# Optimization experiments

Measured on AMD Instinct MI355X. Metric: run time of the kernel, lower is better.

Reference implementation:

```python
import jax, jax.numpy as jnp
import numpy as np
from jax import lax

K = 3      # kernel_size
PAD = 1    # padding
OG = 2     # offset groups


def _conv2d(x, w, b):
    y = lax.conv_general_dilated(x, w, (1, 1), [(PAD, PAD), (PAD, PAD)],
                                 dimension_numbers=('NCHW', 'OIHW', 'NCHW'))
    return y + b[None, :, None, None]


def _deform_conv2d(x, offset, mask, weight):
    # torchvision-style modulated deform_conv2d (v2), stride=1, dilation=1,
    # zero out-of-bounds, offset layout [B, OG*K*K*2, H, W] with (dy, dx) pairs.
    B, C, H, W = x.shape
    O = weight.shape[0]
    K2 = K * K
    Cg = C // OG

    ki, kj = jnp.meshgrid(jnp.arange(K), jnp.arange(K), indexing='ij')
    ki = ki.reshape(K2)
    kj = kj.reshape(K2)
    base_y = jnp.arange(H)[None, :] - PAD + ki[:, None]   # [K2, H]
    base_x = jnp.arange(W)[None, :] - PAD + kj[:, None]   # [K2, W]

    off = offset.reshape(B, OG, K2, 2, H, W)
    py = off[:, :, :, 0] + base_y[None, None, :, :, None].astype(x.dtype)  # [B,OG,K2,H,W]
    px = off[:, :, :, 1] + base_x[None, None, :, None, :].astype(x.dtype)
    m = mask.reshape(B, OG, K2, H, W)

    y0f = jnp.floor(py)
    x0f = jnp.floor(px)
    wy1 = py - y0f   # bilinear weights, grads flow through py/px
    wx1 = px - x0f
    y0 = y0f.astype(jnp.int32)
    x0 = x0f.astype(jnp.int32)
    y1 = y0 + 1
    x1 = x0 + 1

    img = x.reshape(B, OG, Cg, H * W)

    def gather(yi, xi):
        valid = (yi >= 0) & (yi < H) & (xi >= 0) & (xi < W)
        idx = jnp.clip(yi, 0, H - 1) * W + jnp.clip(xi, 0, W - 1)          # [B,OG,K2,H,W]
        v = jnp.take_along_axis(img[:, :, :, None, :],
                                idx.reshape(B, OG, 1, K2, H * W), axis=-1)
        return v.reshape(B, OG, Cg, K2, H, W) * valid[:, :, None].astype(x.dtype)

    v00 = gather(y0, x0)
    v01 = gather(y0, x1)
    v10 = gather(y1, x0)
    v11 = gather(y1, x1)

    wy1e = wy1[:, :, None]   # [B,OG,1,K2,H,W]
    wx1e = wx1[:, :, None]
    val = (v00 * (1 - wy1e) * (1 - wx1e)
           + v01 * (1 - wy1e) * wx1e
           + v10 * wy1e * (1 - wx1e)
           + v11 * wy1e * wx1e)
    val = val * m[:, :, None]                               # modulation mask

    wr = weight.reshape(O, OG, Cg, K2)
    return jnp.einsum('ogck,bgckhw->bohw', wr, val)


def setup_inputs() -> dict:
    key = jax.random.key(0)
    k1, k2, k3, k4, k5 = jax.random.split(key, 5)
    B, C, O, H, W = 4, 64, 64, 128, 128
    K2 = K * K
    x = jax.random.normal(k1, (B, C, H, W), dtype=jnp.float32)
    w_main = jax.random.normal(k2, (O, C, K, K), dtype=jnp.float32) / np.sqrt(C * K2)
    w_off = jax.random.normal(k3, (2 * OG * K2, C, K, K), dtype=jnp.float32) * 0.01
    b_off = jax.random.normal(k4, (2 * OG * K2,), dtype=jnp.float32) * 0.01
    w_mask = jnp.full((OG * K2, C, K, K), 0.5, dtype=jnp.float32)  # init_mask = 0.5
    b_mask = jax.random.normal(k5, (OG * K2,), dtype=jnp.float32) * 0.01
    return {"x": x, "w_main": w_main, "w_off": w_off, "b_off": b_off,
            "w_mask": w_mask, "b_mask": b_mask}


def reference(x, w_main, w_off, b_off, w_mask, b_mask):
    offset = _conv2d(x, w_off, b_off)
    mask = jax.nn.sigmoid(_conv2d(x, w_mask, b_mask))
    return _deform_conv2d(x, offset, mask, w_main)
```

## Files before the change

### kernel.cpp

```cpp
#include <hip/hip_runtime.h>
#include <math.h>

#define BB 4
#define C 64
#define O 64
#define H 128
#define W 128
#define K2 9
#define HW (H*W)
#define NOFF 36

typedef __bf16 bf16;
typedef bf16 bf16x8 __attribute__((ext_vector_type(8)));
typedef float f32x4 __attribute__((ext_vector_type(4)));
typedef unsigned short u16x8 __attribute__((ext_vector_type(8)));
typedef unsigned int u32x4 __attribute__((ext_vector_type(4)));

#define BSTR 55
#define B2STR 19
#define VSTR 36
#define SSTR 72
#define VAL_OFF 14688
#define SMEM_BYTES 28512
#define WFRAG 18432
#define NW_TOTAL 73728

__device__ inline unsigned short f2h_bits(float f) {
  _Float16 h = (_Float16)f;
  return __builtin_bit_cast(unsigned short, h);
}
__device__ inline float h2f(unsigned short u) {
  return (float)__builtin_bit_cast(_Float16, u);
}

__global__ __launch_bounds__(256) void prep_all(
    const float* __restrict__ x, const float* __restrict__ w_main,
    const float* __restrict__ w_off, const float* __restrict__ w_mask,
    unsigned short* __restrict__ xT16, bf16* __restrict__ wfC,
    bf16* __restrict__ wfM) {
  __shared__ float tile[64][68];
  int tid = threadIdx.x;
  int b = blockIdx.x >> 8;
  int p0 = (blockIdx.x & 255) * 64;
#pragma unroll
  for (int it = 0; it < 4; ++it) {
    int c = it * 16 + (tid >> 4);
    int p4 = (tid & 15) * 4;
    *(f32x4*)&tile[c][p4] =
        *(const f32x4*)(x + (size_t)(b * C + c) * HW + p0 + p4);
  }
  __syncthreads();
#pragma unroll
  for (int it = 0; it < 2; ++it) {
    int t = it * 256 + tid;
    int p = t >> 3;
    int h8 = t & 7;
    u16x8 o;
#pragma unroll
    for (int j = 0; j < 8; ++j) {
      bf16 v = (bf16)tile[h8 * 8 + j][p];
      o[j] = __builtin_bit_cast(unsigned short, v);
    }
    *(u16x8*)&xT16[(size_t)(b * HW + p0 + p) * C + h8 * 8] = o;
  }
  int i = blockIdx.x * 256 + tid;
  if (i < NW_TOTAL) {
    int which = (i >= 36864);
    int ii = which ? i - 36864 : i;
    int j = ii & 7;
    int l = (ii >> 3) & 63;
    int rest = ii >> 9;
    int to = rest & 3;
    int kk = (rest >> 2) % 9;
    int ph = (rest >> 2) / 9;
    int m = to * 16 + (l & 15);
    int u = kk * 32 + (l >> 4) * 8 + j;
    int tap = u >> 5;
    int c1 = u & 31;
    if (!which) {
      int c = ph * 32 + c1;
      float v = (m < NOFF) ? w_off[(m * C + c) * K2 + tap]
                : (m < 54) ? w_mask[((m - NOFF) * C + c) * K2 + tap]
                           : 0.f;
      wfC[ii] = (bf16)v;
    } else {
      wfM[ii] = (bf16)w_main[(m * C + ph * 32 + c1) * K2 + tap];
    }
  }
}

__global__ __launch_bounds__(256, 5) void fused_deform(
    const bf16* __restrict__ xT, const bf16* __restrict__ wfC,
    const bf16* __restrict__ wfM, const float* __restrict__ b_off,
    const float* __restrict__ b_mask, float* __restrict__ out) {
  __shared__ __align__(16) char smem[SMEM_BYTES];
  bf16* stage = (bf16*)smem;
  float* bufF = (float*)smem;
  u32x4* buf2 = (u32x4*)smem;
  float* valF = (float*)smem;
  bf16* val = (bf16*)(smem + VAL_OFF);

  const int tid = threadIdx.x;
  const int lane = tid & 63;
  const int wv = tid >> 6;
  const int n16 = lane & 15;
  const int q4 = lane >> 4;
  const int nt = wv & 1;
  const int mh = wv >> 1;
  const int row = nt * 16 + n16;
  const int pg = tid >> 3;
  const int ch = tid & 7;

  const int g8 = blockIdx.x & 7;
  const int slot = blockIdx.x >> 3;
  const int b = g8 >> 1;
  const int ti = (g8 & 1) * 256 + slot;
  const int h0 = ti >> 2;
  const int w0 = (ti & 3) * 32;
  const bf16* xb = xT + (size_t)b * HW * C;

  bf16x8 zero8;
#pragma unroll
  for (int j = 0; j < 8; ++j) zero8[j] = (bf16)0.f;

#pragma unroll
  for (int it = 0; it < 4; ++it) {
    int id = it * 256 + tid;
    if (id < 816) {
      int chk = id & 7;
      int rest = id >> 3;
      int wp = rest % 34;
      int r = rest / 34;
      int yy = h0 + r - 1;
      int xx = w0 + wp - 1;
      bf16x8 v = zero8;
      if ((unsigned)yy < (unsigned)H && (unsigned)xx < (unsigned)W)
        v = *(const bf16x8*)(xb + (size_t)((yy << 7) + xx) * C + chk * 8);
      *(bf16x8*)(stage + (r * 34 + wp) * SSTR + chk * 8) = v;
    }
  }
  __syncthreads();
  f32x4 accC[2] = {{0.f,0.f,0.f,0.f},{0.f,0.f,0.f,0.f}};
#pragma unroll 1
  for (int ph = 0; ph < 2; ++ph) {
#pragma unroll
    for (int kk = 0; kk < 9; ++kk) {
      bf16x8 bfr = *(const bf16x8*)(stage +
          ((kk / 3) * 34 + row + kk % 3) * SSTR + ph * 32 + q4 * 8);
#pragma unroll
      for (int i = 0; i < 2; ++i) {
        int to = 2 * mh + i;
        bf16x8 afr = *(const bf16x8*)(wfC +
            (size_t)(((ph * 9 + kk) * 4 + to) * 64 + lane) * 8);
        accC[i] = __builtin_amdgcn_mfma_f32_16x16x32_bf16(afr, bfr, accC[i], 0, 0, 0);
      }
    }
  }
  __syncthreads();

#pragma unroll
  for (int i = 0; i < 2; ++i)
#pragma unroll
    for (int r = 0; r < 4; ++r) {
      int o = (2 * mh + i) * 16 + q4 * 4 + r;
      float a = accC[i][r];
      if (o < NOFF) {
        bufF[row * BSTR + o] = a + b_off[o];
      } else if (o < 54) {
        float s = a + b_mask[o - NOFF];
        bufF[row * BSTR + o] = 1.f / (1.f + __expf(-s));
      }
    }
  __syncthreads();

  unsigned int rW0[3], rW1[3], rCo[3];
#pragma unroll
  for (int it = 0; it < 3; ++it) {
    int t = it * 256 + tid;
    if (t < 576) {
      int p = t & 31;
      int gk = t >> 5;
      int g = gk / 9, tap = gk % 9;
      float offy = bufF[p * BSTR + 2 * gk];
      float offx = bufF[p * BSTR + 2 * gk + 1];
      float m = bufF[p * BSTR + NOFF + gk];
      float py = offy + (float)(h0 + tap / 3 - 1);
      float px = offx + (float)(w0 + p + tap % 3 - 1);
      float y0f = floorf(py), x0f = floorf(px);
      float wy1 = py - y0f, wx1 = px - x0f;
      float wy0 = 1.f - wy1, wx0 = 1.f - wx1;
      int y0 = (int)y0f, x0 = (int)x0f;
      int y1 = y0 + 1, x1 = x0 + 1;
      bool y0ok = (unsigned)y0 < (unsigned)H, y1ok = (unsigned)y1 < (unsigned)H;
      bool x0ok = (unsigned)x0 < (unsigned)W, x1ok = (unsigned)x1 < (unsigned)W;
      float w00 = (y0ok && x0ok) ? wy0 * wx0 * m : 0.f;
      float w01 = (y0ok && x1ok) ? wy0 * wx1 * m : 0.f;
      float w10 = (y1ok && x0ok) ? wy1 * wx0 * m : 0.f;
      float w11 = (y1ok && x1ok) ? wy1 * wx1 * m : 0.f;
      unsigned int y0c = (unsigned)min(max(y0, 0), H - 1);
      unsigned int y1c = (unsigned)min(max(y1, 0), H - 1);
      unsigned int x0c = (unsigned)min(max(x0, 0), W - 1);
      unsigned int x1c = (unsigned)min(max(x1, 0), W - 1);
      rW0[it] = (unsigned)f2h_bits(w00) | ((unsigned)f2h_bits(w01) << 16);
      rW1[it] = (unsigned)f2h_bits(w10) | ((unsigned)f2h_bits(w11) << 16);
      rCo[it] = y0c | (x0c << 8) | (y1c << 16) | (x1c << 24);
    }
  }
  __syncthreads();
#pragma unroll
  for (int it = 0; it < 3; ++it) {
    int t = it * 256 + tid;
    if (t < 576) {
      int p = t & 31;
      int gk = t >> 5;
      u32x4 pk = {rW0[it], rW1[it], rCo[it], 0u};
      buf2[p * B2STR + gk] = pk;
    }
  }
  __syncthreads();

  f32x4 accM[2] = {{0.f,0.f,0.f,0.f},{0.f,0.f,0.f,0.f}};
  const bf16* bb = xb + ch * 8;
  const int gg = ch >> 2;
#pragma unroll 1
  for (int kc = 0; kc < 3; ++kc) {
    if (kc) __syncthreads();
#pragma unroll
    for (int t = 0; t < 3; ++t) {
      int tap = kc * 3 + t;
      u32x4 t4 = buf2[pg * B2STR + gg * 9 + tap];
      float w00 = h2f(t4.x & 0xffff), w01 = h2f(t4.x >> 16);
      float w10 = h2f(t4.y & 0xffff), w11 = h2f(t4.y >> 16);
      int r0 = (int)(t4.z & 255) << 7;
      int x0 = (int)((t4.z >> 8) & 255);
      int r1 = (int)((t4.z >> 16) & 255) << 7;
      int x1 = (int)(t4.z >> 24);
      bf16x8 v00 = *(const bf16x8*)(bb + (size_t)(r0 + x0) * C);
      bf16x8 v01 = *(const bf16x8*)(bb + (size_t)(r0 + x1) * C);
      bf16x8 v10 = *(const bf16x8*)(bb + (size_t)(r1 + x0) * C);
      bf16x8 v11 = *(const bf16x8*)(bb + (size_t)(r1 + x1) * C);
      bf16x8 res;
#pragma unroll
      for (int j = 0; j < 8; ++j) {
        float v = (float)v00[j] * w00 + (float)v01[j] * w01 +
                  (float)v10[j] * w10 + (float)v11[j] * w11;
        res[j] = (bf16)v;
      }
      *(bf16x8*)(val + (t * 32 + pg) * SSTR + ch * 8) = res;
    }
    __syncthreads();
#pragma unroll
    for (int t = 0; t < 3; ++t) {
      int tap = kc * 3 + t;
#pragma unroll
      for (int g = 0; g < 2; ++g) {
        bf16x8 bfr = *(const bf16x8*)(val +
            (t * 32 + row) * SSTR + g * 32 + q4 * 8);
#pragma unroll
        for (int i = 0; i < 2; ++i) {
          int to = 2 * mh + i;
          bf16x8 afr = *(const bf16x8*)(wfM + (size_t)g * WFRAG +
              (size_t)((tap * 4 + to) * 64 + lane) * 8);
          accM[i] = __builtin_amdgcn_mfma_f32_16x16x32_bf16(afr, bfr, accM[i], 0, 0, 0);
        }
      }
    }
  }

  __syncthreads();
#pragma unroll
  for (int i = 0; i < 2; ++i)
#pragma unroll
    for (int r = 0; r < 4; ++r)
      valF[((2 * mh + i) * 16 + q4 * 4 + r) * VSTR + row] = accM[i][r];
  __syncthreads();
  {
    float* ob = out + (size_t)b * O * HW + (h0 << 7) + w0;
#pragma unroll
    for (int it = 0; it < 2; ++it) {
      int id = it * 256 + tid;
      int o = id >> 3, seg = id & 7;
      f32x4 v = *(f32x4*)&valF[o * VSTR + seg * 4];
      *(f32x4*)&ob[(size_t)o * HW + seg * 4] = v;
    }
  }
}

extern "C" void kernel_launch(void* const* d_in, const int* in_sizes, int n_in,
                              void* d_out, int out_size, void* d_ws,
                              size_t ws_size, hipStream_t stream) {
  const float* x = (const float*)d_in[0];
  const float* w_main = (const float*)d_in[1];
  const float* w_off = (const float*)d_in[2];
  const float* b_off = (const float*)d_in[3];
  const float* w_mask = (const float*)d_in[4];
  const float* b_mask = (const float*)d_in[5];
  float* out = (float*)d_out;

  unsigned short* xT16 = (unsigned short*)d_ws;
  bf16* wfC = (bf16*)(xT16 + (size_t)BB * HW * C);
  bf16* wfM = wfC + 36864;

  prep_all<<<1024, 256, 0, stream>>>(x, w_main, w_off, w_mask, xT16, wfC, wfM);
  fused_deform<<<2048, 256, 0, stream>>>((const bf16*)xT16, wfC, wfM, b_off,
                                         b_mask, out);
}
```

Measured before the change: 115.8 us.

## Shrink shared memory, write outputs directly, and raise occupancy to six blocks

The bilinear tap buffer now lives in its own region after the value staging area, so tap records are written straight to LDS. This removes the register hold and one barrier. The LDS transpose of the output tile is dropped in favour of direct scalar stores from the MFMA accumulators. Together these cut LDS use, which allows launch bounds to rise from five to six blocks per CU. The trade-off is that output stores become 4-byte accesses with 64B contiguity per row instead of 16-byte vector stores, and the new buf2 region must not overlap bufF or stage while they are still live.

```diff
diff --git a/kernel.cpp b/kernel.cpp
--- a/kernel.cpp
+++ b/kernel.cpp
@@ -18,10 +18,9 @@
 
 #define BSTR 55
 #define B2STR 19
-#define VSTR 36
 #define SSTR 72
-#define VAL_OFF 14688
-#define SMEM_BYTES 28512
+#define BUF2_OFF 13824
+#define SMEM_BYTES 23552
 #define WFRAG 18432
 #define NW_TOTAL 73728
 
@@ -89,16 +88,15 @@
   }
 }
 
-__global__ __launch_bounds__(256, 5) void fused_deform(
+__global__ __launch_bounds__(256, 6) void fused_deform(
     const bf16* __restrict__ xT, const bf16* __restrict__ wfC,
     const bf16* __restrict__ wfM, const float* __restrict__ b_off,
     const float* __restrict__ b_mask, float* __restrict__ out) {
   __shared__ __align__(16) char smem[SMEM_BYTES];
   bf16* stage = (bf16*)smem;
   float* bufF = (float*)smem;
-  u32x4* buf2 = (u32x4*)smem;
-  float* valF = (float*)smem;
-  bf16* val = (bf16*)(smem + VAL_OFF);
+  bf16* val = (bf16*)smem;
+  u32x4* buf2 = (u32x4*)(smem + BUF2_OFF);
 
   const int tid = threadIdx.x;
   const int lane = tid & 63;
@@ -173,7 +171,6 @@
     }
   __syncthreads();
 
-  unsigned int rW0[3], rW1[3], rCo[3];
 #pragma unroll
   for (int it = 0; it < 3; ++it) {
     int t = it * 256 + tid;
@@ -201,19 +198,11 @@
       unsigned int y1c = (unsigned)min(max(y1, 0), H - 1);
       unsigned int x0c = (unsigned)min(max(x0, 0), W - 1);
       unsigned int x1c = (unsigned)min(max(x1, 0), W - 1);
-      rW0[it] = (unsigned)f2h_bits(w00) | ((unsigned)f2h_bits(w01) << 16);
-      rW1[it] = (unsigned)f2h_bits(w10) | ((unsigned)f2h_bits(w11) << 16);
-      rCo[it] = y0c | (x0c << 8) | (y1c << 16) | (x1c << 24);
-    }
-  }
-  __syncthreads();
-#pragma unroll
-  for (int it = 0; it < 3; ++it) {
-    int t = it * 256 + tid;
-    if (t < 576) {
-      int p = t & 31;
-      int gk = t >> 5;
-      u32x4 pk = {rW0[it], rW1[it], rCo[it], 0u};
+      u32x4 pk;
+      pk.x = (unsigned)f2h_bits(w00) | ((unsigned)f2h_bits(w01) << 16);
+      pk.y = (unsigned)f2h_bits(w10) | ((unsigned)f2h_bits(w11) << 16);
+      pk.z = y0c | (x0c << 8) | (y1c << 16) | (x1c << 24);
+      pk.w = 0u;
       buf2[p * B2STR + gk] = pk;
     }
   }
@@ -267,22 +256,15 @@
     }
   }
 
-  __syncthreads();
-#pragma unroll
-  for (int i = 0; i < 2; ++i)
-#pragma unroll
-    for (int r = 0; r < 4; ++r)
-      valF[((2 * mh + i) * 16 + q4 * 4 + r) * VSTR + row] = accM[i][r];
-  __syncthreads();
   {
-    float* ob = out + (size_t)b * O * HW + (h0 << 7) + w0;
-#pragma unroll
-    for (int it = 0; it < 2; ++it) {
-      int id = it * 256 + tid;
-      int o = id >> 3, seg = id & 7;
-      f32x4 v = *(f32x4*)&valF[o * VSTR + seg * 4];
-      *(f32x4*)&ob[(size_t)o * HW + seg * 4] = v;
-    }
+    float* ob = out + (size_t)b * O * HW + (h0 << 7) + w0 + row;
+#pragma unroll
+    for (int i = 0; i < 2; ++i)
+#pragma unroll
+      for (int r = 0; r < 4; ++r) {
+        int o = (2 * mh + i) * 16 + q4 * 4 + r;
+        ob[(size_t)o * HW] = accM[i][r];
+      }
   }
 }
 
```

After: 117.3 us. Within noise of the previous version (+1.3%).

## Software-pipeline bilinear gathers across tap chunks and use LDS-only barriers

Applied to the files above, without the earlier changes.

Gathers for the next chunk of three taps are prefetched into registers while the current chunk is interpolated and fed to MFMAs, so global load latency overlaps compute. A lighter barrier waits only on LDS counters (lgkmcnt) instead of all outstanding memory, so pending global prefetches do not stall the barrier. The cost is 12 extra bf16x8 registers per thread, which raises VGPR pressure and may lower occupancy.

```diff
diff --git a/kernel.cpp b/kernel.cpp
--- a/kernel.cpp
+++ b/kernel.cpp
@@ -31,6 +31,12 @@
 }
 __device__ inline float h2f(unsigned short u) {
   return (float)__builtin_bit_cast(_Float16, u);
+}
+
+__device__ inline void bar_lds() {
+  asm volatile("s_waitcnt lgkmcnt(0)" ::: "memory");
+  __builtin_amdgcn_s_barrier();
+  asm volatile("" ::: "memory");
 }
 
 __global__ __launch_bounds__(256) void prep_all(
@@ -222,33 +228,60 @@
   f32x4 accM[2] = {{0.f,0.f,0.f,0.f},{0.f,0.f,0.f,0.f}};
   const bf16* bb = xb + ch * 8;
   const int gg = ch >> 2;
+
+  bf16x8 pre[12];
+  unsigned int pwx[3], pwy[3];
+#pragma unroll
+  for (int t = 0; t < 3; ++t) {
+    u32x4 t4 = buf2[pg * B2STR + gg * 9 + t];
+    pwx[t] = t4.x;
+    pwy[t] = t4.y;
+    int r0 = (int)(t4.z & 255) << 7;
+    int x0 = (int)((t4.z >> 8) & 255);
+    int r1 = (int)((t4.z >> 16) & 255) << 7;
+    int x1 = (int)(t4.z >> 24);
+    pre[t * 4 + 0] = *(const bf16x8*)(bb + (size_t)(r0 + x0) * C);
+    pre[t * 4 + 1] = *(const bf16x8*)(bb + (size_t)(r0 + x1) * C);
+    pre[t * 4 + 2] = *(const bf16x8*)(bb + (size_t)(r1 + x0) * C);
+    pre[t * 4 + 3] = *(const bf16x8*)(bb + (size_t)(r1 + x1) * C);
+  }
 #pragma unroll 1
   for (int kc = 0; kc < 3; ++kc) {
-    if (kc) __syncthreads();
+    bf16x8 res[3];
 #pragma unroll
     for (int t = 0; t < 3; ++t) {
-      int tap = kc * 3 + t;
-      u32x4 t4 = buf2[pg * B2STR + gg * 9 + tap];
-      float w00 = h2f(t4.x & 0xffff), w01 = h2f(t4.x >> 16);
-      float w10 = h2f(t4.y & 0xffff), w11 = h2f(t4.y >> 16);
-      int r0 = (int)(t4.z & 255) << 7;
-      int x0 = (int)((t4.z >> 8) & 255);
-      int r1 = (int)((t4.z >> 16) & 255) << 7;
-      int x1 = (int)(t4.z >> 24);
-      bf16x8 v00 = *(const bf16x8*)(bb + (size_t)(r0 + x0) * C);
-      bf16x8 v01 = *(const bf16x8*)(bb + (size_t)(r0 + x1) * C);
-      bf16x8 v10 = *(const bf16x8*)(bb + (size_t)(r1 + x0) * C);
-      bf16x8 v11 = *(const bf16x8*)(bb + (size_t)(r1 + x1) * C);
-      bf16x8 res;
+      float w00 = h2f(pwx[t] & 0xffff), w01 = h2f(pwx[t] >> 16);
+      float w10 = h2f(pwy[t] & 0xffff), w11 = h2f(pwy[t] >> 16);
+      bf16x8 v00 = pre[t * 4 + 0], v01 = pre[t * 4 + 1];
+      bf16x8 v10 = pre[t * 4 + 2], v11 = pre[t * 4 + 3];
 #pragma unroll
       for (int j = 0; j < 8; ++j) {
         float v = (float)v00[j] * w00 + (float)v01[j] * w01 +
                   (float)v10[j] * w10 + (float)v11[j] * w11;
-        res[j] = (bf16)v;
-      }
-      *(bf16x8*)(val + (t * 32 + pg) * SSTR + ch * 8) = res;
-    }
-    __syncthreads();
+        res[t][j] = (bf16)v;
+      }
+    }
+    if (kc < 2) {
+#pragma unroll
+      for (int t = 0; t < 3; ++t) {
+        u32x4 t4 = buf2[pg * B2STR + gg * 9 + (kc + 1) * 3 + t];
+        pwx[t] = t4.x;
+        pwy[t] = t4.y;
+        int r0 = (int)(t4.z & 255) << 7;
+        int x0 = (int)((t4.z >> 8) & 255);
+        int r1 = (int)((t4.z >> 16) & 255) << 7;
+        int x1 = (int)(t4.z >> 24);
+        pre[t * 4 + 0] = *(const bf16x8*)(bb + (size_t)(r0 + x0) * C);
+        pre[t * 4 + 1] = *(const bf16x8*)(bb + (size_t)(r0 + x1) * C);
+        pre[t * 4 + 2] = *(const bf16x8*)(bb + (size_t)(r1 + x0) * C);
+        pre[t * 4 + 3] = *(const bf16x8*)(bb + (size_t)(r1 + x1) * C);
+      }
+    }
+    if (kc) bar_lds();
+#pragma unroll
+    for (int t = 0; t < 3; ++t)
+      *(bf16x8*)(val + (t * 32 + pg) * SSTR + ch * 8) = res[t];
+    bar_lds();
 #pragma unroll
     for (int t = 0; t < 3; ++t) {
       int tap = kc * 3 + t;
```

After: 174.8 us. +51.0%, slower.

## Software-pipeline deformable gathers one tap-chunk ahead and use LDS-only barriers

Applied to the files above, without the earlier changes.

Prefetches the next three taps' bilinear corner gathers from global memory into registers while the current chunk is interpolated and fed to MFMA. This hides gather latency behind compute. It also replaces __syncthreads with a barrier that waits only on LDS counters, so the in-flight global loads are not drained at each barrier. In exchange it holds 12 extra bf16x8 registers per thread, which may strain the 5-waves launch bound and cause spills.

```diff
diff --git a/kernel.cpp b/kernel.cpp
--- a/kernel.cpp
+++ b/kernel.cpp
@@ -31,6 +31,12 @@
 }
 __device__ inline float h2f(unsigned short u) {
   return (float)__builtin_bit_cast(_Float16, u);
+}
+
+__device__ inline void bar_lds() {
+  asm volatile("s_waitcnt lgkmcnt(0)" ::: "memory");
+  __builtin_amdgcn_s_barrier();
+  asm volatile("" ::: "memory");
 }
 
 __global__ __launch_bounds__(256) void prep_all(
@@ -88,6 +94,32 @@
     }
   }
 }
+
+#define LOADTAP(GK, WX, WY, V0, V1, V2, V3)                    \
+  do {                                                         \
+    u32x4 t4 = buf2[pg * B2STR + (GK)];                        \
+    WX = t4.x;                                                 \
+    WY = t4.y;                                                 \
+    int r0 = (int)(t4.z & 255) << 7;                           \
+    int x0 = (int)((t4.z >> 8) & 255);                         \
+    int r1 = (int)((t4.z >> 16) & 255) << 7;                   \
+    int x1 = (int)(t4.z >> 24);                                \
+    V0 = *(const bf16x8*)(bb + (size_t)(r0 + x0) * C);         \
+    V1 = *(const bf16x8*)(bb + (size_t)(r0 + x1) * C);         \
+    V2 = *(const bf16x8*)(bb + (size_t)(r1 + x0) * C);         \
+    V3 = *(const bf16x8*)(bb + (size_t)(r1 + x1) * C);         \
+  } while (0)
+
+#define LERP(WX, WY, V0, V1, V2, V3, DST)                           \
+  do {                                                              \
+    float w00 = h2f(WX & 0xffff), w01 = h2f(WX >> 16);              \
+    float w10 = h2f(WY & 0xffff), w11 = h2f(WY >> 16);              \
+    _Pragma("unroll") for (int j = 0; j < 8; ++j) {                 \
+      float v = (float)V0[j] * w00 + (float)V1[j] * w01 +           \
+                (float)V2[j] * w10 + (float)V3[j] * w11;            \
+      DST[j] = (bf16)v;                                             \
+    }                                                               \
+  } while (0)
 
 __global__ __launch_bounds__(256, 5) void fused_deform(
     const bf16* __restrict__ xT, const bf16* __restrict__ wfC,
@@ -222,33 +254,30 @@
   f32x4 accM[2] = {{0.f,0.f,0.f,0.f},{0.f,0.f,0.f,0.f}};
   const bf16* bb = xb + ch * 8;
   const int gg = ch >> 2;
+
+  bf16x8 a00, a01, a10, a11, b00c, b01c, b10c, b11c, c00, c01, c10, c11;
+  unsigned int qw0x, qw0y, qw1x, qw1y, qw2x, qw2y;
+  LOADTAP(gg * 9 + 0, qw0x, qw0y, a00, a01, a10, a11);
+  LOADTAP(gg * 9 + 1, qw1x, qw1y, b00c, b01c, b10c, b11c);
+  LOADTAP(gg * 9 + 2, qw2x, qw2y, c00, c01, c10, c11);
+
 #pragma unroll 1
   for (int kc = 0; kc < 3; ++kc) {
-    if (kc) __syncthreads();
-#pragma unroll
-    for (int t = 0; t < 3; ++t) {
-      int tap = kc * 3 + t;
-      u32x4 t4 = buf2[pg * B2STR + gg * 9 + tap];
-      float w00 = h2f(t4.x & 0xffff), w01 = h2f(t4.x >> 16);
-      float w10 = h2f(t4.y & 0xffff), w11 = h2f(t4.y >> 16);
-      int r0 = (int)(t4.z & 255) << 7;
-      int x0 = (int)((t4.z >> 8) & 255);
-      int r1 = (int)((t4.z >> 16) & 255) << 7;
-      int x1 = (int)(t4.z >> 24);
-      bf16x8 v00 = *(const bf16x8*)(bb + (size_t)(r0 + x0) * C);
-      bf16x8 v01 = *(const bf16x8*)(bb + (size_t)(r0 + x1) * C);
-      bf16x8 v10 = *(const bf16x8*)(bb + (size_t)(r1 + x0) * C);
-      bf16x8 v11 = *(const bf16x8*)(bb + (size_t)(r1 + x1) * C);
-      bf16x8 res;
-#pragma unroll
-      for (int j = 0; j < 8; ++j) {
-        float v = (float)v00[j] * w00 + (float)v01[j] * w01 +
-                  (float)v10[j] * w10 + (float)v11[j] * w11;
-        res[j] = (bf16)v;
-      }
-      *(bf16x8*)(val + (t * 32 + pg) * SSTR + ch * 8) = res;
-    }
-    __syncthreads();
+    bf16x8 r0v, r1v, r2v;
+    LERP(qw0x, qw0y, a00, a01, a10, a11, r0v);
+    LERP(qw1x, qw1y, b00c, b01c, b10c, b11c, r1v);
+    LERP(qw2x, qw2y, c00, c01, c10, c11, r2v);
+    if (kc < 2) {
+      int base = gg * 9 + (kc + 1) * 3;
+      LOADTAP(base + 0, qw0x, qw0y, a00, a01, a10, a11);
+      LOADTAP(base + 1, qw1x, qw1y, b00c, b01c, b10c, b11c);
+      LOADTAP(base + 2, qw2x, qw2y, c00, c01, c10, c11);
+    }
+    if (kc) bar_lds();
+    *(bf16x8*)(val + (0 * 32 + pg) * SSTR + ch * 8) = r0v;
+    *(bf16x8*)(val + (1 * 32 + pg) * SSTR + ch * 8) = r1v;
+    *(bf16x8*)(val + (2 * 32 + pg) * SSTR + ch * 8) = r2v;
+    bar_lds();
 #pragma unroll
     for (int t = 0; t < 3; ++t) {
       int tap = kc * 3 + t;
```

New measurement: 176.0 us. +52.0%, slower.
